# Kernel optimization log

Measured on AMD Instinct MI355X. Metric: run time of the kernel, lower is better.

The kernel has to match this reference:

```python
import jax, jax.numpy as jnp
import numpy as np

N_NODES = 50000
N_PAIRS = 200000
HID1 = 256
HID2 = 32


def gcn_conv(x, src, dst, W, b, n):
    # PyG GCNConv: project, add self-loops, sym-normalize, scatter-add to dst.
    sl = jnp.arange(n, dtype=src.dtype)
    s = jnp.concatenate([src, sl])
    d = jnp.concatenate([dst, sl])
    deg = jnp.zeros((n,), x.dtype).at[d].add(1.0)
    dinv = jax.lax.rsqrt(deg)  # deg >= 1 due to self-loops
    xw = x @ W  # [n, out]
    msg = xw[s] * (dinv[s] * dinv[d])[:, None]  # [E+n, out]
    out = jax.ops.segment_sum(msg, d, num_segments=n)
    return out + b


def setup_inputs() -> dict:
    key = jax.random.key(0)
    ks = jax.random.split(key, 16)
    inp = {
        "x": jax.random.randint(ks[0], (N_NODES,), 0, N_NODES),
        "edge1": jax.random.randint(ks[1], (2, 1600000), 0, N_NODES),
        "pos": jax.random.randint(ks[2], (N_PAIRS, 2), 0, N_NODES),
        "idx": jax.random.randint(ks[3], (N_PAIRS,), 0, N_PAIRS),
        "ei2": jax.random.randint(ks[4], (2, 1600000), 0, N_PAIRS),
        "emb_table": jax.random.normal(ks[5], (N_NODES + 1, HID1), jnp.float32) * 0.02,
        "W1": jax.random.normal(ks[6], (HID1, HID2), jnp.float32) * (1.0 / np.sqrt(HID1)),
        "b1": jnp.zeros((HID2,), jnp.float32),
        "W2a": jax.random.normal(ks[7], (HID2, HID2), jnp.float32) * (1.0 / np.sqrt(HID2)),
        "b2a": jnp.zeros((HID2,), jnp.float32),
        "W2b": jax.random.normal(ks[8], (HID2, HID2), jnp.float32) * (1.0 / np.sqrt(HID2)),
        "b2b": jnp.zeros((HID2,), jnp.float32),
        "Wp": jax.random.normal(ks[9], (HID2, 1), jnp.float32) * (1.0 / np.sqrt(HID2)),
        "bp": jnp.zeros((1,), jnp.float32),
    }
    return inp


def reference(x, edge1, pos, idx, ei2, emb_table, W1, b1, W2a, b2a, W2b, b2b, Wp, bp):
    # eval mode: all Dropouts are identity; no LayerNorm/GraphNorm (default flags False)
    h = emb_table[x]  # [N, HID1] embedding lookup (squeeze is no-op for 1D ids)
    # conv1s: single GCNConv HID1 -> HID2 + ReLU
    h = jax.nn.relu(gcn_conv(h, edge1[0], edge1[1], W1, b1, N_NODES))
    # pairwise gather-multiply over pos
    h = h[pos[:, 0]] * h[pos[:, 1]]  # [M, HID2]
    # conv2s / conv2s_r on the pair graph (edge2 = ei2, edge2_r = flipped)
    h = (jax.nn.relu(gcn_conv(h, ei2[0], ei2[1], W2a, b2a, N_PAIRS))
         + jax.nn.relu(gcn_conv(h, ei2[1], ei2[0], W2b, b2b, N_PAIRS)))
    # gather by idx, then multiply consecutive (even, odd) rows
    h = h[idx]  # [2Q, HID2]
    h = h[0::2] * h[1::2]  # [Q, HID2]
    return h @ Wp + bp  # [Q, 1]
```

## Files before the change

kernel.cpp:

```cpp
#include <hip/hip_runtime.h>
#include <hip/hip_fp16.h>
#include <math.h>


#define SL     256
#define SLOG   8
#define SL1    64
#define SLOG1  6
#define CAP    2432
#define SHIFT  18
#define NMASK  ((1 << SHIFT) - 1)
#define BCH    8192
#define BT     1024
#define EPT    8
#define MAXSL2 1024
#define PB     64
#define EROW   264

typedef short bf16x8 __attribute__((ext_vector_type(8)));
typedef float f32x4 __attribute__((ext_vector_type(4)));

static __device__ __forceinline__ unsigned short f2bf(float f) {
    union { float f; unsigned u; } v;
    v.f = f;
    unsigned r = v.u + 0x7FFF + ((v.u >> 16) & 1);
    return (unsigned short)(r >> 16);
}
static __device__ __forceinline__ float bf2f(unsigned short h) {
    return __uint_as_float(((unsigned)h) << 16);
}
static __device__ __forceinline__ float bflo(unsigned u) { return __uint_as_float(u << 16); }
static __device__ __forceinline__ float bfhi(unsigned u) { return __uint_as_float(u & 0xFFFF0000u); }

static __device__ __forceinline__ float4 bfacc(float4 a, uint2 w) {
    a.x += bflo(w.x);
    a.y += bfhi(w.x);
    a.z += bflo(w.y);
    a.w += bfhi(w.y);
    return a;
}
static __device__ __forceinline__ float4 hacc(float4 a, uint2 w) {
    float2 f0 = __half22float2(*(__half2*)&w.x);
    float2 f1 = __half22float2(*(__half2*)&w.y);
    a.x += f0.x;
    a.y += f0.y;
    a.z += f1.x;
    a.w += f1.y;
    return a;
}
static __device__ __forceinline__ float4 h2f4(uint2 w) {
    float2 f0 = __half22float2(*(__half2*)&w.x);
    float2 f1 = __half22float2(*(__half2*)&w.y);
    float4 r = {f0.x, f0.y, f1.x, f1.y};
    return r;
}
static __device__ __forceinline__ uint2 f42h(float4 f) {
    __half2 h0 = __floats2half2_rn(f.x, f.y);
    __half2 h1 = __floats2half2_rn(f.z, f.w);
    uint2 r = {*(unsigned*)&h0, *(unsigned*)&h1};
    return r;
}

__global__ __launch_bounds__(256) void k_init(int* __restrict__ bumpF,
                                              int* __restrict__ bumpR,
                                              int* __restrict__ bump1,
                                              int NS2, int NS1) {
    int i = blockIdx.x * 256 + threadIdx.x;
    if (i < NS2) {
        bumpF[i] = i * CAP;
        bumpR[i] = i * CAP;
    }
    if (i < NS1) bump1[i] = i * CAP;
}

__global__ __launch_bounds__(BT) void k_build(const int* __restrict__ s2,
                                              const int* __restrict__ d2,
                                              const int* __restrict__ s1,
                                              const int* __restrict__ d1,
                                              int* bumpF, int* bumpR, int* bump1,
                                              int* __restrict__ bktF,
                                              int* __restrict__ bktR,
                                              int* __restrict__ bkt1,
                                              const float* __restrict__ W1,
                                              const float* __restrict__ W2a,
                                              const float* __restrict__ W2b,
                                              unsigned short* __restrict__ Wbhi,
                                              unsigned short* __restrict__ Wblo,
                                              unsigned short* __restrict__ W2ah,
                                              unsigned short* __restrict__ W2al,
                                              unsigned short* __restrict__ W2bh,
                                              unsigned short* __restrict__ W2bl,
                                              int E2, int E1, int NS2, int NS1,
                                              int NB2, int NB1) {
    __shared__ int stag[BCH];
    __shared__ unsigned short stag2[BCH];
    __shared__ int lbF[MAXSL2];
    __shared__ int lbR[MAXSL2];
    __shared__ int bgF[MAXSL2], bgR[MAXSL2];
    __shared__ int wsum[BT / 64];
    int tid = threadIdx.x, bid = blockIdx.x;
    int lane = tid & 63, wid = tid >> 6;

    auto exscan = [&](int v) -> int {
        int sc = v;
#pragma unroll
        for (int d = 1; d < 64; d <<= 1) {
            int t = __shfl_up(sc, d, 64);
            if (lane >= d) sc += t;
        }
        if (lane == 63) wsum[wid] = sc;
        __syncthreads();
        int woff = 0;
        for (int w2 = 0; w2 < wid; w2++) woff += wsum[w2];
        __syncthreads();
        return woff + sc - v;
    };

    if (bid < NB2) {
        if (tid < NS2) { lbF[tid] = 0; lbR[tid] = 0; }
        __syncthreads();
        int eb = bid * BCH;
        int n = E2 - eb; if (n > BCH) n = BCH;
        int sv[EPT], dv[EPT], ofF[EPT], ofR[EPT];
#pragma unroll
        for (int k = 0; k < EPT; k++) {
            int i = k * BT + tid;
            if (i < n) {
                sv[k] = s2[eb + i];
                dv[k] = d2[eb + i];
                ofF[k] = atomicAdd(&lbF[dv[k] >> SLOG], 1);
                ofR[k] = atomicAdd(&lbR[sv[k] >> SLOG], 1);
            }
        }
        __syncthreads();
        int cF = (tid < NS2) ? lbF[tid] : 0;
        int cR = (tid < NS2) ? lbR[tid] : 0;
        int preF = exscan(cF);
        int preR = exscan(cR);
        if (tid < NS2) {
            lbF[tid] = preF;
            lbR[tid] = preR;
            bgF[tid] = cF ? atomicAdd(&bumpF[tid], cF) : 0;
            bgR[tid] = cR ? atomicAdd(&bumpR[tid], cR) : 0;
        }
        __syncthreads();
#pragma unroll
        for (int k = 0; k < EPT; k++) {
            int i = k * BT + tid;
            if (i < n) {
                int sf = dv[k] >> SLOG;
                int p = lbF[sf] + ofF[k];
                stag[p] = ((dv[k] & (SL - 1)) << SHIFT) | sv[k];
                stag2[p] = (unsigned short)sf;
            }
        }
        __syncthreads();
        for (int i = tid; i < n; i += BT) {
            int sf = stag2[i];
            int gp = bgF[sf] + (i - lbF[sf]);
            if (gp < (sf + 1) * CAP) bktF[gp] = stag[i];
        }
        __syncthreads();
#pragma unroll
        for (int k = 0; k < EPT; k++) {
            int i = k * BT + tid;
            if (i < n) {
                int sr = sv[k] >> SLOG;
                int p = lbR[sr] + ofR[k];
                stag[p] = ((sv[k] & (SL - 1)) << SHIFT) | dv[k];
                stag2[p] = (unsigned short)sr;
            }
        }
        __syncthreads();
        for (int i = tid; i < n; i += BT) {
            int sr = stag2[i];
            int gp = bgR[sr] + (i - lbR[sr]);
            if (gp < (sr + 1) * CAP) bktR[gp] = stag[i];
        }
    } else if (bid < NB2 + NB1) {
        if (tid < NS1) lbF[tid] = 0;
        __syncthreads();
        int eb = (bid - NB2) * BCH;
        int n = E1 - eb; if (n > BCH) n = BCH;
        int sv[EPT], dv[EPT], of[EPT];
#pragma unroll
        for (int k = 0; k < EPT; k++) {
            int i = k * BT + tid;
            if (i < n) {
                sv[k] = s1[eb + i];
                dv[k] = d1[eb + i];
                of[k] = atomicAdd(&lbF[dv[k] >> SLOG1], 1);
            }
        }
        __syncthreads();
        int c = (tid < NS1) ? lbF[tid] : 0;
        int pre = exscan(c);
        if (tid < NS1) {
            lbF[tid] = pre;
            bgF[tid] = c ? atomicAdd(&bump1[tid], c) : 0;
        }
        __syncthreads();
#pragma unroll
        for (int k = 0; k < EPT; k++) {
            int i = k * BT + tid;
            if (i < n) {
                int sf = dv[k] >> SLOG1;
                int p = lbF[sf] + of[k];
                stag[p] = ((dv[k] & (SL1 - 1)) << SHIFT) | sv[k];
                stag2[p] = (unsigned short)sf;
            }
        }
        __syncthreads();
        for (int i = tid; i < n; i += BT) {
            int sf = stag2[i];
            int gp = bgF[sf] + (i - lbF[sf]);
            if (gp < (sf + 1) * CAP) bkt1[gp] = stag[i];
        }
    } else {
        int i = (bid - NB2 - NB1) * BT + tid;
        if (i < 8192) {
            int k = i >> 5, c = i & 31;
            float w = W1[i];
            unsigned short hi = f2bf(w);
            unsigned short lo = f2bf(w - bf2f(hi));
            Wbhi[c * 256 + k] = hi;
            Wblo[c * 256 + k] = lo;
        }
        if (i < 1024) {
            int k = i >> 5, c = i & 31;
            float wa = W2a[i], wb = W2b[i];
            unsigned short ha = f2bf(wa);
            unsigned short hb = f2bf(wb);
            W2ah[c * 32 + k] = ha;
            W2al[c * 32 + k] = f2bf(wa - bf2f(ha));
            W2bh[c * 32 + k] = hb;
            W2bl[c * 32 + k] = f2bf(wb - bf2f(hb));
        }
    }
}

__global__ __launch_bounds__(256) void k_sort(int* __restrict__ bkt1, const int* __restrict__ bump1,
                                              float* __restrict__ dinv1, int* __restrict__ beg1,
                                              int* __restrict__ cnt1,
                                              int* __restrict__ bktF, const int* __restrict__ bumpF,
                                              float* __restrict__ dinvF, int* __restrict__ begF,
                                              int* __restrict__ cntF,
                                              int* __restrict__ bktR, const int* __restrict__ bumpR,
                                              float* __restrict__ dinvR, int* __restrict__ begR,
                                              int* __restrict__ cntR,
                                              int NS1, int NS2, int N1, int NP) {
    __shared__ int A[CAP];
    __shared__ int S[CAP];
    __shared__ int hN[SL], hD[SL];
    __shared__ int wsum[4];
    int bid = blockIdx.x, tid = threadIdx.x;
    int s, sls, N;
    int* bkt;
    const int* bump;
    float* dinv;
    int* beg;
    int* cntA;
    if (bid < NS1) {
        s = bid;
        bkt = bkt1; bump = bump1; dinv = dinv1; beg = beg1; cntA = cnt1;
        sls = SL1; N = N1;
    } else if (bid < NS1 + NS2) {
        s = bid - NS1;
        bkt = bktF; bump = bumpF; dinv = dinvF; beg = begF; cntA = cntF;
        sls = SL; N = NP;
    } else {
        s = bid - NS1 - NS2;
        bkt = bktR; bump = bumpR; dinv = dinvR; beg = begR; cntA = cntR;
        sls = SL; N = NP;
    }
    hN[tid] = 0;
    hD[tid] = 0;
    __syncthreads();
    int cnt = bump[s] - s * CAP;
    if (cnt > CAP) cnt = CAP;
    int* b = bkt + (size_t)s * CAP;
    for (int i = tid; i < cnt; i += 256) {
        int e = b[i];
        atomicAdd(&hN[(e & NMASK) >> 10], 1);
        atomicAdd(&hD[e >> SHIFT], 1);
    }
    __syncthreads();
    int cn = hN[tid];
    int cd = hD[tid];
    int lane = tid & 63, wid = tid >> 6;
    auto exscan = [&](int v) -> int {
        int sc = v;
#pragma unroll
        for (int d = 1; d < 64; d <<= 1) {
            int t = __shfl_up(sc, d, 64);
            if (lane >= d) sc += t;
        }
        if (lane == 63) wsum[wid] = sc;
        __syncthreads();
        int woff = 0;
        for (int w = 0; w < wid; w++) woff += wsum[w];
        __syncthreads();
        return woff + sc - v;
    };
    int preN = exscan(cn);
    int preD = exscan(cd);
    hN[tid] = preN;
    hD[tid] = preD;
    if (tid < sls) {
        int v = s * sls + tid;
        if (v < N) {
            dinv[v] = 1.f / sqrtf((float)cd + 1.f);
            beg[v] = s * CAP + preD;
            cntA[v] = cd;
        }
    }
    __syncthreads();
    for (int i = tid; i < cnt; i += 256) {
        int e = b[i];
        int p = atomicAdd(&hN[(e & NMASK) >> 10], 1);
        A[p] = e;
    }
    __syncthreads();
    for (int i = tid; i < cnt; i += 256) {
        int e = A[i];
        int p = atomicAdd(&hD[e >> SHIFT], 1);
        S[p] = e & NMASK;
    }
    __syncthreads();
    for (int i = tid; i < cnt; i += 256) b[i] = S[i];
}

__global__ __launch_bounds__(256) void k_xw1(const int* __restrict__ x,
                                             const float* __restrict__ emb,
                                             const unsigned short* __restrict__ Wbhi,
                                             const unsigned short* __restrict__ Wblo,
                                             const float* __restrict__ dinv1,
                                             __half* __restrict__ y1, int N) {
    __shared__ unsigned short sEhi[32 * EROW];
    __shared__ unsigned short sElo[32 * EROW];
    int tid = threadIdx.x;
    int lane = tid & 63, wv = tid >> 6;
    int r0 = blockIdx.x * 32;
    const float4* emb4 = (const float4*)emb;
#pragma unroll
    for (int p = 0; p < 8; p++) {
        int row = p * 4 + wv;
        int r = r0 + row;
        int xr = x[(r < N) ? r : 0];
        float4 e = emb4[(size_t)xr * 64 + lane];
        unsigned short h0 = f2bf(e.x), h1 = f2bf(e.y), h2 = f2bf(e.z), h3 = f2bf(e.w);
        ushort4 hi = {h0, h1, h2, h3};
        ushort4 lo = {f2bf(e.x - bf2f(h0)), f2bf(e.y - bf2f(h1)),
                      f2bf(e.z - bf2f(h2)), f2bf(e.w - bf2f(h3))};
        *(ushort4*)&sEhi[row * EROW + lane * 4] = hi;
        *(ushort4*)&sElo[row * EROW + lane * 4] = lo;
    }
    __syncthreads();
    int col = lane & 15, quad = lane >> 4;
    int rowtile = wv >> 1, ntile = wv & 1;
    f32x4 acc = {0.f, 0.f, 0.f, 0.f};
    const unsigned short* arow_hi = &sEhi[(rowtile * 16 + col) * EROW + quad * 8];
    const unsigned short* arow_lo = &sElo[(rowtile * 16 + col) * EROW + quad * 8];
    const unsigned short* bh = Wbhi + (ntile * 16 + col) * 256 + quad * 8;
    const unsigned short* bl = Wblo + (ntile * 16 + col) * 256 + quad * 8;
#pragma unroll
    for (int kb = 0; kb < 256; kb += 32) {
        bf16x8 ahi = *(const bf16x8*)(arow_hi + kb);
        bf16x8 alo = *(const bf16x8*)(arow_lo + kb);
        bf16x8 bhv = *(const bf16x8*)(bh + kb);
        bf16x8 blv = *(const bf16x8*)(bl + kb);
        acc = __builtin_amdgcn_mfma_f32_16x16x32_bf16(ahi, bhv, acc, 0, 0, 0);
        acc = __builtin_amdgcn_mfma_f32_16x16x32_bf16(alo, bhv, acc, 0, 0, 0);
        acc = __builtin_amdgcn_mfma_f32_16x16x32_bf16(ahi, blv, acc, 0, 0, 0);
    }
#pragma unroll
    for (int reg = 0; reg < 4; reg++) {
        int grow = r0 + rowtile * 16 + quad * 4 + reg;
        if (grow < N) {
            float dv = dinv1[grow];
            y1[grow * 32 + ntile * 16 + col] = __float2half(acc[reg] * dv);
        }
    }
}

static __device__ __forceinline__ float4 gcn_sum_h8(const int* __restrict__ adj, int bg, int end,
                                                    const uint2* __restrict__ y2, int q,
                                                    float4 acc) {
    float4 a1 = {0.f, 0.f, 0.f, 0.f};
    int i = bg;
    for (; i + 8 <= end; i += 8) {
        int u0 = adj[i], u1 = adj[i + 1], u2 = adj[i + 2], u3 = adj[i + 3];
        int u4 = adj[i + 4], u5 = adj[i + 5], u6 = adj[i + 6], u7 = adj[i + 7];
        uint2 w0 = y2[u0 * 8 + q];
        uint2 w1 = y2[u1 * 8 + q];
        uint2 w2 = y2[u2 * 8 + q];
        uint2 w3 = y2[u3 * 8 + q];
        uint2 w4 = y2[u4 * 8 + q];
        uint2 w5 = y2[u5 * 8 + q];
        uint2 w6 = y2[u6 * 8 + q];
        uint2 w7 = y2[u7 * 8 + q];
        acc = hacc(acc, w0);
        a1 = hacc(a1, w1);
        acc = hacc(acc, w2);
        a1 = hacc(a1, w3);
        acc = hacc(acc, w4);
        a1 = hacc(a1, w5);
        acc = hacc(acc, w6);
        a1 = hacc(a1, w7);
    }
    for (; i + 4 <= end; i += 4) {
        int u0 = adj[i], u1 = adj[i + 1], u2 = adj[i + 2], u3 = adj[i + 3];
        uint2 w0 = y2[u0 * 8 + q];
        uint2 w1 = y2[u1 * 8 + q];
        uint2 w2 = y2[u2 * 8 + q];
        uint2 w3 = y2[u3 * 8 + q];
        acc = hacc(acc, w0);
        a1 = hacc(a1, w1);
        acc = hacc(acc, w2);
        a1 = hacc(a1, w3);
    }
    for (; i < end; i++) acc = hacc(acc, y2[adj[i] * 8 + q]);
    acc.x += a1.x;
    acc.y += a1.y;
    acc.z += a1.z;
    acc.w += a1.w;
    return acc;
}

static __device__ __forceinline__ float4 gcn_sum_bf(const int* __restrict__ adj, int bg, int end,
                                                    const uint2* __restrict__ y2, int q,
                                                    float4 acc) {
    float4 a1 = {0.f, 0.f, 0.f, 0.f};
    int i = bg;
    for (; i + 4 <= end; i += 4) {
        int u0 = adj[i], u1 = adj[i + 1], u2 = adj[i + 2], u3 = adj[i + 3];
        uint2 w0 = y2[u0 * 8 + q];
        uint2 w1 = y2[u1 * 8 + q];
        uint2 w2 = y2[u2 * 8 + q];
        uint2 w3 = y2[u3 * 8 + q];
        acc = bfacc(acc, w0);
        a1 = bfacc(a1, w1);
        acc = bfacc(acc, w2);
        a1 = bfacc(a1, w3);
    }
    for (; i < end; i++) acc = bfacc(acc, y2[adj[i] * 8 + q]);
    acc.x += a1.x;
    acc.y += a1.y;
    acc.z += a1.z;
    acc.w += a1.w;
    return acc;
}

__global__ __launch_bounds__(256) void k_gath1(const int* __restrict__ adj,
                                               const int* __restrict__ beg,
                                               const int* __restrict__ cntA,
                                               const float* __restrict__ dinv,
                                               const __half* __restrict__ y1,
                                               __half* __restrict__ out1, int N) {
    int gid = blockIdx.x * 256 + threadIdx.x;
    int v = gid >> 3, q = gid & 7;
    if (v >= N) return;
    int bg = beg[v];
    int end = bg + cntA[v];
    float dv = dinv[v];
    const uint2* y2 = (const uint2*)y1;
    float4 acc = {0.f, 0.f, 0.f, 0.f};
    acc = hacc(acc, y2[v * 8 + q]);
    acc = gcn_sum_h8(adj, bg, end, y2, q, acc);
    acc.x *= dv;
    acc.y *= dv;
    acc.z *= dv;
    acc.w *= dv;
    ((uint2*)out1)[v * 8 + q] = f42h(acc);
}

__global__ __launch_bounds__(256) void k_gath2(const int* __restrict__ adjF,
                                               const int* __restrict__ begF,
                                               const int* __restrict__ cntF,
                                               const float* __restrict__ dinvF,
                                               const unsigned short* __restrict__ ya,
                                               const int* __restrict__ adjR,
                                               const int* __restrict__ begR,
                                               const int* __restrict__ cntR,
                                               const float* __restrict__ dinvR,
                                               const unsigned short* __restrict__ yb,
                                               const float* __restrict__ b2a,
                                               const float* __restrict__ b2b,
                                               __half* __restrict__ h3, int N) {
    int gid = blockIdx.x * 256 + threadIdx.x;
    int v = gid >> 3, q = gid & 7;
    if (v >= N) return;
    const uint2* ya2 = (const uint2*)ya;
    const uint2* yb2 = (const uint2*)yb;
    float4 aF = {0.f, 0.f, 0.f, 0.f};
    aF = bfacc(aF, ya2[v * 8 + q]);
    int bF = begF[v];
    aF = gcn_sum_bf(adjF, bF, bF + cntF[v], ya2, q, aF);
    float4 aR = {0.f, 0.f, 0.f, 0.f};
    aR = bfacc(aR, yb2[v * 8 + q]);
    int bR = begR[v];
    aR = gcn_sum_bf(adjR, bR, bR + cntR[v], yb2, q, aR);
    float dvF = dinvF[v], dvR = dinvR[v];
    float4 ba = ((const float4*)b2a)[q];
    float4 bb = ((const float4*)b2b)[q];
    float4 h;
    h.x = fmaxf(fmaf(aF.x, dvF, ba.x), 0.f) + fmaxf(fmaf(aR.x, dvR, bb.x), 0.f);
    h.y = fmaxf(fmaf(aF.y, dvF, ba.y), 0.f) + fmaxf(fmaf(aR.y, dvR, bb.y), 0.f);
    h.z = fmaxf(fmaf(aF.z, dvF, ba.z), 0.f) + fmaxf(fmaf(aR.z, dvR, bb.z), 0.f);
    h.w = fmaxf(fmaf(aF.w, dvF, ba.w), 0.f) + fmaxf(fmaf(aR.w, dvR, bb.w), 0.f);
    ((uint2*)h3)[v * 8 + q] = f42h(h);
}

__global__ __launch_bounds__(256) void k_xw2(const int* __restrict__ pos,
                                             const __half* __restrict__ out1,
                                             const float* __restrict__ b1,
                                             const unsigned short* __restrict__ W2ah,
                                             const unsigned short* __restrict__ W2al,
                                             const unsigned short* __restrict__ W2bh,
                                             const unsigned short* __restrict__ W2bl,
                                             const float* __restrict__ dinvF,
                                             const float* __restrict__ dinvR,
                                             unsigned short* __restrict__ ya,
                                             unsigned short* __restrict__ yb,
                                             int NP) {
    __shared__ unsigned short sHhi[PB * 32];
    __shared__ unsigned short sHlo[PB * 32];
    __shared__ int sPos[PB * 2];
    int tid = threadIdx.x;
    int p0 = blockIdx.x * PB;
    if (tid < PB * 2) {
        int gi = p0 * 2 + tid;
        sPos[tid] = (gi < NP * 2) ? pos[gi] : 0;
    }
    __syncthreads();
    const uint2* o12 = (const uint2*)out1;
    int q = tid & 7;
    float4 bq = ((const float4*)b1)[q];
#pragma unroll
    for (int half = 0; half < 2; half++) {
        int p = half * 32 + (tid >> 3);
        int ra = sPos[2 * p] * 8, rb = sPos[2 * p + 1] * 8;
        float4 ea = h2f4(o12[ra + q]);
        float4 eb = h2f4(o12[rb + q]);
        float4 h;
        h.x = fmaxf(ea.x + bq.x, 0.f) * fmaxf(eb.x + bq.x, 0.f);
        h.y = fmaxf(ea.y + bq.y, 0.f) * fmaxf(eb.y + bq.y, 0.f);
        h.z = fmaxf(ea.z + bq.z, 0.f) * fmaxf(eb.z + bq.z, 0.f);
        h.w = fmaxf(ea.w + bq.w, 0.f) * fmaxf(eb.w + bq.w, 0.f);
        unsigned short h0 = f2bf(h.x), h1 = f2bf(h.y), h2 = f2bf(h.z), h3 = f2bf(h.w);
        ushort4 hi = {h0, h1, h2, h3};
        ushort4 lo = {f2bf(h.x - bf2f(h0)), f2bf(h.y - bf2f(h1)),
                      f2bf(h.z - bf2f(h2)), f2bf(h.w - bf2f(h3))};
        *(ushort4*)&sHhi[p * 32 + q * 4] = hi;
        *(ushort4*)&sHlo[p * 32 + q * 4] = lo;
    }
    __syncthreads();
    int lane = tid & 63, wv = tid >> 6;
    int col = lane & 15, quad = lane >> 4;
    bf16x8 ahi = *(const bf16x8*)&sHhi[(wv * 16 + col) * 32 + quad * 8];
    bf16x8 alo = *(const bf16x8*)&sHlo[(wv * 16 + col) * 32 + quad * 8];
    f32x4 accA[2], accB[2];
#pragma unroll
    for (int nt = 0; nt < 2; nt++) {
        int off = (nt * 16 + col) * 32 + quad * 8;
        bf16x8 bah = *(const bf16x8*)(W2ah + off);
        bf16x8 bal = *(const bf16x8*)(W2al + off);
        bf16x8 bbh = *(const bf16x8*)(W2bh + off);
        bf16x8 bbl = *(const bf16x8*)(W2bl + off);
        f32x4 z = {0.f, 0.f, 0.f, 0.f};
        f32x4 a = __builtin_amdgcn_mfma_f32_16x16x32_bf16(ahi, bah, z, 0, 0, 0);
        a = __builtin_amdgcn_mfma_f32_16x16x32_bf16(alo, bah, a, 0, 0, 0);
        a = __builtin_amdgcn_mfma_f32_16x16x32_bf16(ahi, bal, a, 0, 0, 0);
        accA[nt] = a;
        f32x4 b = __builtin_amdgcn_mfma_f32_16x16x32_bf16(ahi, bbh, z, 0, 0, 0);
        b = __builtin_amdgcn_mfma_f32_16x16x32_bf16(alo, bbh, b, 0, 0, 0);
        b = __builtin_amdgcn_mfma_f32_16x16x32_bf16(ahi, bbl, b, 0, 0, 0);
        accB[nt] = b;
    }
#pragma unroll
    for (int reg = 0; reg < 4; reg++) {
        int p = wv * 16 + quad * 4 + reg;
        int pg = p0 + p;
        if (pg < NP) {
            float dA = dinvF[pg], dB = dinvR[pg];
#pragma unroll
            for (int nt = 0; nt < 2; nt++) {
                ya[pg * 32 + nt * 16 + col] = f2bf(accA[nt][reg] * dA);
                yb[pg * 32 + nt * 16 + col] = f2bf(accB[nt][reg] * dB);
            }
        }
    }
}

__global__ __launch_bounds__(256) void k_final(const int* __restrict__ idx,
                                               const __half* __restrict__ h3,
                                               const float* __restrict__ Wp,
                                               const float* __restrict__ bp,
                                               float* __restrict__ out, int Q) {
    int gid = blockIdx.x * 256 + threadIdx.x;
    int qi = gid >> 3, q = gid & 7;
    if (qi >= Q) return;
    int i0 = idx[2 * qi] * 8, i1 = idx[2 * qi + 1] * 8;
    float4 wp = ((const float4*)Wp)[q];
    const uint2* H = (const uint2*)h3;
    float4 h0 = h2f4(H[i0 + q]), h1 = h2f4(H[i1 + q]);
    float s = h0.x * h1.x * wp.x + h0.y * h1.y * wp.y + h0.z * h1.z * wp.z + h0.w * h1.w * wp.w;
    s += __shfl_xor(s, 1);
    s += __shfl_xor(s, 2);
    s += __shfl_xor(s, 4);
    if (q == 0) out[qi] = s + bp[0];
}

extern "C" void kernel_launch(void* const* d_in, const int* in_sizes, int n_in,
                              void* d_out, int out_size, void* d_ws, size_t ws_size,
                              hipStream_t stream) {
    const int* x    = (const int*)d_in[0];
    const int* e1   = (const int*)d_in[1];
    const int* pos  = (const int*)d_in[2];
    const int* idx  = (const int*)d_in[3];
    const int* e2   = (const int*)d_in[4];
    const float* emb = (const float*)d_in[5];
    const float* W1  = (const float*)d_in[6];
    const float* b1  = (const float*)d_in[7];
    const float* W2a = (const float*)d_in[8];
    const float* b2a = (const float*)d_in[9];
    const float* W2b = (const float*)d_in[10];
    const float* b2b = (const float*)d_in[11];
    const float* Wp  = (const float*)d_in[12];
    const float* bp  = (const float*)d_in[13];

    const int N1 = in_sizes[0];
    const int E1 = in_sizes[1] / 2;
    const int NP = in_sizes[3];
    const int E2 = in_sizes[4] / 2;
    const int Q  = out_size;
    (void)n_in; (void)ws_size;

    const int NS1 = (N1 + SL1 - 1) >> SLOG1;
    const int NS2 = (NP + SL - 1) >> SLOG;

    char* w = (char*)d_ws;
    size_t o = 0;
    auto alloc = [&](size_t bytes) { size_t r = o; o += (bytes + 255) & ~(size_t)255; return r; };
    float* dinv1  = (float*)(w + alloc((size_t)(N1 + 2 * NP) * 4));
    float* dinv2f = dinv1 + N1;
    float* dinv2r = dinv2f + NP;
    int* beg1  = (int*)(w + alloc((size_t)(N1 + 2 * NP) * 4));
    int* beg2f = beg1 + N1;
    int* beg2r = beg2f + NP;
    int* cnt1  = (int*)(w + alloc((size_t)(N1 + 2 * NP) * 4));
    int* cnt2f = cnt1 + N1;
    int* cnt2r = cnt2f + NP;
    int* bumpF = (int*)(w + alloc((size_t)(2 * NS2 + NS1) * 4));
    int* bumpR = bumpF + NS2;
    int* bump1 = bumpR + NS2;
    unsigned short* Wbhi = (unsigned short*)(w + alloc(8192 * 2));
    unsigned short* Wblo = (unsigned short*)(w + alloc(8192 * 2));
    unsigned short* W2ah = (unsigned short*)(w + alloc(1024 * 2));
    unsigned short* W2al = (unsigned short*)(w + alloc(1024 * 2));
    unsigned short* W2bh = (unsigned short*)(w + alloc(1024 * 2));
    unsigned short* W2bl = (unsigned short*)(w + alloc(1024 * 2));
    int* bktF = (int*)(w + alloc((size_t)NS2 * CAP * 4));
    int* bktR = (int*)(w + alloc((size_t)NS2 * CAP * 4));
    int* bkt1 = (int*)(w + alloc((size_t)NS1 * CAP * 4));
    __half* out1 = (__half*)(w + alloc((size_t)N1 * 32 * 2));
    __half* y1   = (__half*)(w + alloc((size_t)N1 * 32 * 2));
    unsigned short* ya = (unsigned short*)(w + alloc((size_t)NP * 32 * 2));
    unsigned short* yb = (unsigned short*)(w + alloc((size_t)NP * 32 * 2));
    __half* h3  = (__half*)(w + alloc((size_t)NP * 32 * 2));

    const int B = 256;
    auto cdiv = [](long long a, long long b) { return (int)((a + b - 1) / b); };
    const int NB2 = cdiv(E2, BCH), NB1 = cdiv(E1, BCH);
    const int NBW = cdiv(8192, BT);

    k_init<<<cdiv(NS2 > NS1 ? NS2 : NS1, B), B, 0, stream>>>(bumpF, bumpR, bump1, NS2, NS1);
    k_build<<<NB2 + NB1 + NBW, BT, 0, stream>>>(e2, e2 + E2, e1, e1 + E1,
                                                bumpF, bumpR, bump1, bktF, bktR, bkt1,
                                                W1, W2a, W2b, Wbhi, Wblo,
                                                W2ah, W2al, W2bh, W2bl,
                                                E2, E1, NS2, NS1, NB2, NB1);
    k_sort<<<NS1 + 2 * NS2, B, 0, stream>>>(bkt1, bump1, dinv1, beg1, cnt1,
                                            bktF, bumpF, dinv2f, beg2f, cnt2f,
                                            bktR, bumpR, dinv2r, beg2r, cnt2r,
                                            NS1, NS2, N1, NP);
    k_xw1<<<cdiv(N1, 32), B, 0, stream>>>(x, emb, Wbhi, Wblo, dinv1, y1, N1);
    k_gath1<<<cdiv((long long)N1 * 8, B), B, 0, stream>>>(bkt1, beg1, cnt1, dinv1, y1, out1, N1);
    k_xw2<<<cdiv(NP, PB), B, 0, stream>>>(pos, out1, b1, W2ah, W2al, W2bh, W2bl,
                                          dinv2f, dinv2r, ya, yb, NP);
    k_gath2<<<cdiv((long long)NP * 8, B), B, 0, stream>>>(bktF, beg2f, cnt2f, dinv2f, ya,
                                                          bktR, beg2r, cnt2r, dinv2r, yb,
                                                          b2a, b2b, h3, NP);
    k_final<<<cdiv((long long)Q * 8, B), B, 0, stream>>>(idx, h3, Wp, bp, (float*)d_out, Q);
}
```

Before: 280.0 us.

## Fuse bucket sort into gather kernels, keep sorted adjacency in LDS

The separate sort kernel, which wrote sorted adjacency back to global memory, becomes a degree-only histogram kernel that computes dinv. The full two-pass counting sort now runs inside the gather kernels (k_SG1, k_SG2), with 512 threads per slice and the adjacency kept in shared memory. This removes the global write and re-read of the sorted buckets and the beg/cnt arrays. In exchange, each bucket is read twice (once for degrees, once in the gather), and the pair-graph kernel has far fewer blocks with serialized forward and reverse sorts, which may lower occupancy and latency hiding.

```diff
diff --git a/kernel.cpp b/kernel.cpp
--- a/kernel.cpp
+++ b/kernel.cpp
@@ -16,6 +16,7 @@
 #define MAXSL2 1024
 #define PB     64
 #define EROW   264
+#define SGT    512
 
 typedef short bf16x8 __attribute__((ext_vector_type(8)));
 typedef float f32x4 __attribute__((ext_vector_type(4)));
@@ -239,95 +240,37 @@
     }
 }
 
-__global__ __launch_bounds__(256) void k_sort(int* __restrict__ bkt1, const int* __restrict__ bump1,
-                                              float* __restrict__ dinv1, int* __restrict__ beg1,
-                                              int* __restrict__ cnt1,
-                                              int* __restrict__ bktF, const int* __restrict__ bumpF,
-                                              float* __restrict__ dinvF, int* __restrict__ begF,
-                                              int* __restrict__ cntF,
-                                              int* __restrict__ bktR, const int* __restrict__ bumpR,
-                                              float* __restrict__ dinvR, int* __restrict__ begR,
-                                              int* __restrict__ cntR,
-                                              int NS1, int NS2, int N1, int NP) {
-    __shared__ int A[CAP];
-    __shared__ int S[CAP];
-    __shared__ int hN[SL], hD[SL];
-    __shared__ int wsum[4];
+__global__ __launch_bounds__(256) void k_sortD(const int* __restrict__ bkt1, const int* __restrict__ bump1,
+                                               float* __restrict__ dinv1,
+                                               const int* __restrict__ bktF, const int* __restrict__ bumpF,
+                                               float* __restrict__ dinvF,
+                                               const int* __restrict__ bktR, const int* __restrict__ bumpR,
+                                               float* __restrict__ dinvR,
+                                               int NS1, int NS2, int N1, int NP) {
+    __shared__ int hist[SL];
     int bid = blockIdx.x, tid = threadIdx.x;
     int s, sls, N;
-    int* bkt;
+    const int* bkt;
     const int* bump;
     float* dinv;
-    int* beg;
-    int* cntA;
     if (bid < NS1) {
-        s = bid;
-        bkt = bkt1; bump = bump1; dinv = dinv1; beg = beg1; cntA = cnt1;
-        sls = SL1; N = N1;
+        s = bid; bkt = bkt1; bump = bump1; dinv = dinv1; sls = SL1; N = N1;
     } else if (bid < NS1 + NS2) {
-        s = bid - NS1;
-        bkt = bktF; bump = bumpF; dinv = dinvF; beg = begF; cntA = cntF;
-        sls = SL; N = NP;
+        s = bid - NS1; bkt = bktF; bump = bumpF; dinv = dinvF; sls = SL; N = NP;
     } else {
-        s = bid - NS1 - NS2;
-        bkt = bktR; bump = bumpR; dinv = dinvR; beg = begR; cntA = cntR;
-        sls = SL; N = NP;
-    }
-    hN[tid] = 0;
-    hD[tid] = 0;
+        s = bid - NS1 - NS2; bkt = bktR; bump = bumpR; dinv = dinvR; sls = SL; N = NP;
+    }
+    hist[tid] = 0;
     __syncthreads();
     int cnt = bump[s] - s * CAP;
     if (cnt > CAP) cnt = CAP;
-    int* b = bkt + (size_t)s * CAP;
-    for (int i = tid; i < cnt; i += 256) {
-        int e = b[i];
-        atomicAdd(&hN[(e & NMASK) >> 10], 1);
-        atomicAdd(&hD[e >> SHIFT], 1);
-    }
-    __syncthreads();
-    int cn = hN[tid];
-    int cd = hD[tid];
-    int lane = tid & 63, wid = tid >> 6;
-    auto exscan = [&](int v) -> int {
-        int sc = v;
-#pragma unroll
-        for (int d = 1; d < 64; d <<= 1) {
-            int t = __shfl_up(sc, d, 64);
-            if (lane >= d) sc += t;
-        }
-        if (lane == 63) wsum[wid] = sc;
-        __syncthreads();
-        int woff = 0;
-        for (int w = 0; w < wid; w++) woff += wsum[w];
-        __syncthreads();
-        return woff + sc - v;
-    };
-    int preN = exscan(cn);
-    int preD = exscan(cd);
-    hN[tid] = preN;
-    hD[tid] = preD;
+    const int* b = bkt + (size_t)s * CAP;
+    for (int i = tid; i < cnt; i += 256) atomicAdd(&hist[b[i] >> SHIFT], 1);
+    __syncthreads();
     if (tid < sls) {
         int v = s * sls + tid;
-        if (v < N) {
-            dinv[v] = 1.f / sqrtf((float)cd + 1.f);
-            beg[v] = s * CAP + preD;
-            cntA[v] = cd;
-        }
-    }
-    __syncthreads();
-    for (int i = tid; i < cnt; i += 256) {
-        int e = b[i];
-        int p = atomicAdd(&hN[(e & NMASK) >> 10], 1);
-        A[p] = e;
-    }
-    __syncthreads();
-    for (int i = tid; i < cnt; i += 256) {
-        int e = A[i];
-        int p = atomicAdd(&hD[e >> SHIFT], 1);
-        S[p] = e & NMASK;
-    }
-    __syncthreads();
-    for (int i = tid; i < cnt; i += 256) b[i] = S[i];
+        if (v < N) dinv[v] = 1.f / sqrtf((float)hist[tid] + 1.f);
+    }
 }
 
 __global__ __launch_bounds__(256) void k_xw1(const int* __restrict__ x,
@@ -383,14 +326,76 @@
     }
 }
 
-static __device__ __forceinline__ float4 gcn_sum_h8(const int* __restrict__ adj, int bg, int end,
-                                                    const uint2* __restrict__ y2, int q,
-                                                    float4 acc) {
-    float4 a1 = {0.f, 0.f, 0.f, 0.f};
+__global__ __launch_bounds__(SGT) void k_SG1(const int* __restrict__ bkt1,
+                                             const int* __restrict__ bump1,
+                                             const float* __restrict__ dinv1,
+                                             const __half* __restrict__ y1,
+                                             __half* __restrict__ out1, int N1) {
+    __shared__ int S[CAP];
+    __shared__ int As[CAP];
+    __shared__ int hN[SGT], hD[SGT];
+    __shared__ int begD[SL1], cntD[SL1];
+    __shared__ int wsum[SGT / 64];
+    int s = blockIdx.x, tid = threadIdx.x;
+    int lane = tid & 63, wid = tid >> 6;
+    auto exscan = [&](int v) -> int {
+        int sc = v;
+#pragma unroll
+        for (int d = 1; d < 64; d <<= 1) {
+            int t = __shfl_up(sc, d, 64);
+            if (lane >= d) sc += t;
+        }
+        if (lane == 63) wsum[wid] = sc;
+        __syncthreads();
+        int woff = 0;
+        for (int w = 0; w < wid; w++) woff += wsum[w];
+        __syncthreads();
+        return woff + sc - v;
+    };
+    hN[tid] = 0;
+    hD[tid] = 0;
+    __syncthreads();
+    int cnt = bump1[s] - s * CAP;
+    if (cnt > CAP) cnt = CAP;
+    const int* b = bkt1 + (size_t)s * CAP;
+    for (int i = tid; i < cnt; i += SGT) {
+        int e = b[i];
+        As[i] = e;
+        atomicAdd(&hN[(e & NMASK) >> 10], 1);
+        atomicAdd(&hD[e >> SHIFT], 1);
+    }
+    __syncthreads();
+    int cn = hN[tid], cd = hD[tid];
+    int preN = exscan(cn);
+    int preD = exscan(cd);
+    hN[tid] = preN;
+    hD[tid] = preD;
+    if (tid < SL1) { begD[tid] = preD; cntD[tid] = cd; }
+    __syncthreads();
+    for (int i = tid; i < cnt; i += SGT) {
+        int e = As[i];
+        int p = atomicAdd(&hN[(e & NMASK) >> 10], 1);
+        S[p] = e;
+    }
+    __syncthreads();
+    for (int i = tid; i < cnt; i += SGT) {
+        int e = S[i];
+        int p = atomicAdd(&hD[e >> SHIFT], 1);
+        As[p] = e & NMASK;
+    }
+    __syncthreads();
+    int vl = tid >> 3, q = tid & 7;
+    int v = s * SL1 + vl;
+    if (v >= N1) return;
+    const uint2* y2 = (const uint2*)y1;
+    int bg = begD[vl], end = bg + cntD[vl];
+    float dv = dinv1[v];
+    float4 acc = {0.f, 0.f, 0.f, 0.f}, a1 = {0.f, 0.f, 0.f, 0.f};
+    acc = hacc(acc, y2[v * 8 + q]);
     int i = bg;
     for (; i + 8 <= end; i += 8) {
-        int u0 = adj[i], u1 = adj[i + 1], u2 = adj[i + 2], u3 = adj[i + 3];
-        int u4 = adj[i + 4], u5 = adj[i + 5], u6 = adj[i + 6], u7 = adj[i + 7];
+        int u0 = As[i], u1 = As[i + 1], u2 = As[i + 2], u3 = As[i + 3];
+        int u4 = As[i + 4], u5 = As[i + 5], u6 = As[i + 6], u7 = As[i + 7];
         uint2 w0 = y2[u0 * 8 + q];
         uint2 w1 = y2[u1 * 8 + q];
         uint2 w2 = y2[u2 * 8 + q];
@@ -409,7 +414,7 @@
         a1 = hacc(a1, w7);
     }
     for (; i + 4 <= end; i += 4) {
-        int u0 = adj[i], u1 = adj[i + 1], u2 = adj[i + 2], u3 = adj[i + 3];
+        int u0 = As[i], u1 = As[i + 1], u2 = As[i + 2], u3 = As[i + 3];
         uint2 w0 = y2[u0 * 8 + q];
         uint2 w1 = y2[u1 * 8 + q];
         uint2 w2 = y2[u2 * 8 + q];
@@ -419,54 +424,11 @@
         acc = hacc(acc, w2);
         a1 = hacc(a1, w3);
     }
-    for (; i < end; i++) acc = hacc(acc, y2[adj[i] * 8 + q]);
+    for (; i < end; i++) acc = hacc(acc, y2[As[i] * 8 + q]);
     acc.x += a1.x;
     acc.y += a1.y;
     acc.z += a1.z;
     acc.w += a1.w;
-    return acc;
-}
-
-static __device__ __forceinline__ float4 gcn_sum_bf(const int* __restrict__ adj, int bg, int end,
-                                                    const uint2* __restrict__ y2, int q,
-                                                    float4 acc) {
-    float4 a1 = {0.f, 0.f, 0.f, 0.f};
-    int i = bg;
-    for (; i + 4 <= end; i += 4) {
-        int u0 = adj[i], u1 = adj[i + 1], u2 = adj[i + 2], u3 = adj[i + 3];
-        uint2 w0 = y2[u0 * 8 + q];
-        uint2 w1 = y2[u1 * 8 + q];
-        uint2 w2 = y2[u2 * 8 + q];
-        uint2 w3 = y2[u3 * 8 + q];
-        acc = bfacc(acc, w0);
-        a1 = bfacc(a1, w1);
-        acc = bfacc(acc, w2);
-        a1 = bfacc(a1, w3);
-    }
-    for (; i < end; i++) acc = bfacc(acc, y2[adj[i] * 8 + q]);
-    acc.x += a1.x;
-    acc.y += a1.y;
-    acc.z += a1.z;
-    acc.w += a1.w;
-    return acc;
-}
-
-__global__ __launch_bounds__(256) void k_gath1(const int* __restrict__ adj,
-                                               const int* __restrict__ beg,
-                                               const int* __restrict__ cntA,
-                                               const float* __restrict__ dinv,
-                                               const __half* __restrict__ y1,
-                                               __half* __restrict__ out1, int N) {
-    int gid = blockIdx.x * 256 + threadIdx.x;
-    int v = gid >> 3, q = gid & 7;
-    if (v >= N) return;
-    int bg = beg[v];
-    int end = bg + cntA[v];
-    float dv = dinv[v];
-    const uint2* y2 = (const uint2*)y1;
-    float4 acc = {0.f, 0.f, 0.f, 0.f};
-    acc = hacc(acc, y2[v * 8 + q]);
-    acc = gcn_sum_h8(adj, bg, end, y2, q, acc);
     acc.x *= dv;
     acc.y *= dv;
     acc.z *= dv;
@@ -474,41 +436,144 @@
     ((uint2*)out1)[v * 8 + q] = f42h(acc);
 }
 
-__global__ __launch_bounds__(256) void k_gath2(const int* __restrict__ adjF,
-                                               const int* __restrict__ begF,
-                                               const int* __restrict__ cntF,
-                                               const float* __restrict__ dinvF,
-                                               const unsigned short* __restrict__ ya,
-                                               const int* __restrict__ adjR,
-                                               const int* __restrict__ begR,
-                                               const int* __restrict__ cntR,
-                                               const float* __restrict__ dinvR,
-                                               const unsigned short* __restrict__ yb,
-                                               const float* __restrict__ b2a,
-                                               const float* __restrict__ b2b,
-                                               __half* __restrict__ h3, int N) {
-    int gid = blockIdx.x * 256 + threadIdx.x;
-    int v = gid >> 3, q = gid & 7;
-    if (v >= N) return;
+__global__ __launch_bounds__(SGT) void k_SG2(const int* __restrict__ bktF,
+                                             const int* __restrict__ bumpF,
+                                             const float* __restrict__ dinvF,
+                                             const unsigned short* __restrict__ ya,
+                                             const int* __restrict__ bktR,
+                                             const int* __restrict__ bumpR,
+                                             const float* __restrict__ dinvR,
+                                             const unsigned short* __restrict__ yb,
+                                             const float* __restrict__ b2a,
+                                             const float* __restrict__ b2b,
+                                             __half* __restrict__ h3, int NP) {
+    __shared__ int S[CAP];
+    __shared__ int As[CAP];
+    __shared__ int hN[SGT], hD[SGT];
+    __shared__ int begD[SL], cntD[SL];
+    __shared__ int wsum[SGT / 64];
+    int s = blockIdx.x, tid = threadIdx.x;
+    int lane = tid & 63, wid = tid >> 6;
+    auto exscan = [&](int v) -> int {
+        int sc = v;
+#pragma unroll
+        for (int d = 1; d < 64; d <<= 1) {
+            int t = __shfl_up(sc, d, 64);
+            if (lane >= d) sc += t;
+        }
+        if (lane == 63) wsum[wid] = sc;
+        __syncthreads();
+        int woff = 0;
+        for (int w = 0; w < wid; w++) woff += wsum[w];
+        __syncthreads();
+        return woff + sc - v;
+    };
+    auto sort_slice = [&](const int* bkt, const int* bump) {
+        hN[tid] = 0;
+        hD[tid] = 0;
+        __syncthreads();
+        int cnt = bump[s] - s * CAP;
+        if (cnt > CAP) cnt = CAP;
+        const int* b = bkt + (size_t)s * CAP;
+        for (int i = tid; i < cnt; i += SGT) {
+            int e = b[i];
+            As[i] = e;
+            atomicAdd(&hN[(e & NMASK) >> 10], 1);
+            atomicAdd(&hD[e >> SHIFT], 1);
+        }
+        __syncthreads();
+        int cn = hN[tid], cd = hD[tid];
+        int preN = exscan(cn);
+        int preD = exscan(cd);
+        hN[tid] = preN;
+        hD[tid] = preD;
+        if (tid < SL) { begD[tid] = preD; cntD[tid] = cd; }
+        __syncthreads();
+        for (int i = tid; i < cnt; i += SGT) {
+            int e = As[i];
+            int p = atomicAdd(&hN[(e & NMASK) >> 10], 1);
+            S[p] = e;
+        }
+        __syncthreads();
+        for (int i = tid; i < cnt; i += SGT) {
+            int e = S[i];
+            int p = atomicAdd(&hD[e >> SHIFT], 1);
+            As[p] = e & NMASK;
+        }
+        __syncthreads();
+    };
+    sort_slice(bktF, bumpF);
     const uint2* ya2 = (const uint2*)ya;
+    float4 accF[4];
+#pragma unroll
+    for (int it = 0; it < 4; it++) {
+        int item = it * SGT + tid;
+        int vl = item >> 3, q = item & 7;
+        int v = s * SL + vl;
+        float4 acc = {0.f, 0.f, 0.f, 0.f};
+        if (v < NP) {
+            float4 a1 = {0.f, 0.f, 0.f, 0.f};
+            acc = bfacc(acc, ya2[v * 8 + q]);
+            int i = begD[vl], end = i + cntD[vl];
+            for (; i + 4 <= end; i += 4) {
+                int u0 = As[i], u1 = As[i + 1], u2 = As[i + 2], u3 = As[i + 3];
+                uint2 w0 = ya2[u0 * 8 + q];
+                uint2 w1 = ya2[u1 * 8 + q];
+                uint2 w2 = ya2[u2 * 8 + q];
+                uint2 w3 = ya2[u3 * 8 + q];
+                acc = bfacc(acc, w0);
+                a1 = bfacc(a1, w1);
+                acc = bfacc(acc, w2);
+                a1 = bfacc(a1, w3);
+            }
+            for (; i < end; i++) acc = bfacc(acc, ya2[As[i] * 8 + q]);
+            acc.x += a1.x;
+            acc.y += a1.y;
+            acc.z += a1.z;
+            acc.w += a1.w;
+        }
+        accF[it] = acc;
+    }
+    __syncthreads();
+    sort_slice(bktR, bumpR);
     const uint2* yb2 = (const uint2*)yb;
-    float4 aF = {0.f, 0.f, 0.f, 0.f};
-    aF = bfacc(aF, ya2[v * 8 + q]);
-    int bF = begF[v];
-    aF = gcn_sum_bf(adjF, bF, bF + cntF[v], ya2, q, aF);
-    float4 aR = {0.f, 0.f, 0.f, 0.f};
-    aR = bfacc(aR, yb2[v * 8 + q]);
-    int bR = begR[v];
-    aR = gcn_sum_bf(adjR, bR, bR + cntR[v], yb2, q, aR);
-    float dvF = dinvF[v], dvR = dinvR[v];
-    float4 ba = ((const float4*)b2a)[q];
-    float4 bb = ((const float4*)b2b)[q];
-    float4 h;
-    h.x = fmaxf(fmaf(aF.x, dvF, ba.x), 0.f) + fmaxf(fmaf(aR.x, dvR, bb.x), 0.f);
-    h.y = fmaxf(fmaf(aF.y, dvF, ba.y), 0.f) + fmaxf(fmaf(aR.y, dvR, bb.y), 0.f);
-    h.z = fmaxf(fmaf(aF.z, dvF, ba.z), 0.f) + fmaxf(fmaf(aR.z, dvR, bb.z), 0.f);
-    h.w = fmaxf(fmaf(aF.w, dvF, ba.w), 0.f) + fmaxf(fmaf(aR.w, dvR, bb.w), 0.f);
-    ((uint2*)h3)[v * 8 + q] = f42h(h);
+#pragma unroll
+    for (int it = 0; it < 4; it++) {
+        int item = it * SGT + tid;
+        int vl = item >> 3, q = item & 7;
+        int v = s * SL + vl;
+        if (v < NP) {
+            float4 aR = {0.f, 0.f, 0.f, 0.f}, a1 = {0.f, 0.f, 0.f, 0.f};
+            aR = bfacc(aR, yb2[v * 8 + q]);
+            int i = begD[vl], end = i + cntD[vl];
+            for (; i + 4 <= end; i += 4) {
+                int u0 = As[i], u1 = As[i + 1], u2 = As[i + 2], u3 = As[i + 3];
+                uint2 w0 = yb2[u0 * 8 + q];
+                uint2 w1 = yb2[u1 * 8 + q];
+                uint2 w2 = yb2[u2 * 8 + q];
+                uint2 w3 = yb2[u3 * 8 + q];
+                aR = bfacc(aR, w0);
+                a1 = bfacc(a1, w1);
+                aR = bfacc(aR, w2);
+                a1 = bfacc(a1, w3);
+            }
+            for (; i < end; i++) aR = bfacc(aR, yb2[As[i] * 8 + q]);
+            aR.x += a1.x;
+            aR.y += a1.y;
+            aR.z += a1.z;
+            aR.w += a1.w;
+            float dvF = dinvF[v], dvR = dinvR[v];
+            float4 ba = ((const float4*)b2a)[q];
+            float4 bb = ((const float4*)b2b)[q];
+            float4 aF = accF[it];
+            float4 h;
+            h.x = fmaxf(fmaf(aF.x, dvF, ba.x), 0.f) + fmaxf(fmaf(aR.x, dvR, bb.x), 0.f);
+            h.y = fmaxf(fmaf(aF.y, dvF, ba.y), 0.f) + fmaxf(fmaf(aR.y, dvR, bb.y), 0.f);
+            h.z = fmaxf(fmaf(aF.z, dvF, ba.z), 0.f) + fmaxf(fmaf(aR.z, dvR, bb.z), 0.f);
+            h.w = fmaxf(fmaf(aF.w, dvF, ba.w), 0.f) + fmaxf(fmaf(aR.w, dvR, bb.w), 0.f);
+            ((uint2*)h3)[v * 8 + q] = f42h(h);
+        }
+    }
 }
 
 __global__ __launch_bounds__(256) void k_xw2(const int* __restrict__ pos,
@@ -645,12 +710,6 @@
     float* dinv1  = (float*)(w + alloc((size_t)(N1 + 2 * NP) * 4));
     float* dinv2f = dinv1 + N1;
     float* dinv2r = dinv2f + NP;
-    int* beg1  = (int*)(w + alloc((size_t)(N1 + 2 * NP) * 4));
-    int* beg2f = beg1 + N1;
-    int* beg2r = beg2f + NP;
-    int* cnt1  = (int*)(w + alloc((size_t)(N1 + 2 * NP) * 4));
-    int* cnt2f = cnt1 + N1;
-    int* cnt2r = cnt2f + NP;
     int* bumpF = (int*)(w + alloc((size_t)(2 * NS2 + NS1) * 4));
     int* bumpR = bumpF + NS2;
     int* bump1 = bumpR + NS2;
@@ -680,16 +739,16 @@
                                                 W1, W2a, W2b, Wbhi, Wblo,
                                                 W2ah, W2al, W2bh, W2bl,
                                                 E2, E1, NS2, NS1, NB2, NB1);
-    k_sort<<<NS1 + 2 * NS2, B, 0, stream>>>(bkt1, bump1, dinv1, beg1, cnt1,
-                                            bktF, bumpF, dinv2f, beg2f, cnt2f,
-                                            bktR, bumpR, dinv2r, beg2r, cnt2r,
-                                            NS1, NS2, N1, NP);
+    k_sortD<<<NS1 + 2 * NS2, B, 0, stream>>>(bkt1, bump1, dinv1,
+                                             bktF, bumpF, dinv2f,
+                                             bktR, bumpR, dinv2r,
+                                             NS1, NS2, N1, NP);
     k_xw1<<<cdiv(N1, 32), B, 0, stream>>>(x, emb, Wbhi, Wblo, dinv1, y1, N1);
-    k_gath1<<<cdiv((long long)N1 * 8, B), B, 0, stream>>>(bkt1, beg1, cnt1, dinv1, y1, out1, N1);
+    k_SG1<<<NS1, SGT, 0, stream>>>(bkt1, bump1, dinv1, y1, out1, N1);
     k_xw2<<<cdiv(NP, PB), B, 0, stream>>>(pos, out1, b1, W2ah, W2al, W2bh, W2bl,
                                           dinv2f, dinv2r, ya, yb, NP);
-    k_gath2<<<cdiv((long long)NP * 8, B), B, 0, stream>>>(bktF, beg2f, cnt2f, dinv2f, ya,
-                                                          bktR, beg2r, cnt2r, dinv2r, yb,
-                                                          b2a, b2b, h3, NP);
+    k_SG2<<<NS2, SGT, 0, stream>>>(bktF, bumpF, dinv2f, ya,
+                                   bktR, bumpR, dinv2r, yb,
+                                   b2a, b2b, h3, NP);
     k_final<<<cdiv((long long)Q * 8, B), B, 0, stream>>>(idx, h3, Wp, bp, (float*)d_out, Q);
 }
```

New measurement: 291.9 us. +4.2%, slower.
